# Optimization experiments

Measured on AMD Instinct MI355X. Metric: run time of the kernel, lower is better.

Reference implementation:

```python
import jax, jax.numpy as jnp
import numpy as np

NUM_EMBEDDINGS = 1024
EMBEDDING_DIM = 64
COMMITMENT_COST = 0.25


def setup_inputs() -> dict:
    key = jax.random.key(0)
    k1, k2 = jax.random.split(key)
    inputs = jax.random.normal(k1, (64, 32, 32, EMBEDDING_DIM), dtype=jnp.float32)
    # matches nn.Embedding weight init: uniform(-1/K, 1/K)
    codebook = jax.random.uniform(
        k2, (NUM_EMBEDDINGS, EMBEDDING_DIM), dtype=jnp.float32,
        minval=-1.0 / NUM_EMBEDDINGS, maxval=1.0 / NUM_EMBEDDINGS)
    return {"inputs": inputs, "codebook": codebook}


def reference(inputs, codebook):
    input_shape = inputs.shape
    flat = inputs.reshape(-1, EMBEDDING_DIM)  # [N, D]
    distances = (jnp.sum(flat * flat, axis=1, keepdims=True)
                 + jnp.sum(codebook * codebook, axis=1)
                 - 2.0 * jnp.matmul(flat, codebook.T))
    encoding_indices = jnp.argmin(distances, axis=1)  # [N]
    quantized = codebook[encoding_indices].reshape(input_shape)
    codebook_loss = jnp.mean((jax.lax.stop_gradient(quantized) - inputs) ** 2)
    commitment_loss = jnp.mean((jax.lax.stop_gradient(inputs) - quantized) ** 2)
    vq_loss = codebook_loss + COMMITMENT_COST * commitment_loss
    # straight-through estimator
    quantized_st = inputs + jax.lax.stop_gradient(quantized - inputs)
    return quantized_st, vq_loss
```

## Files before the change

kernel.cpp:

```cpp
#include <hip/hip_runtime.h>

typedef __attribute__((ext_vector_type(8))) short short8;
typedef __attribute__((ext_vector_type(4))) float f32x4;
typedef __attribute__((ext_vector_type(4))) unsigned short u16x4;

#define NVEC 65536
#define DDIM 64
#define KCODES 1024
#define NELEM 4194304
#define VPB 128

static __device__ inline unsigned short f2bf(float f) {
  unsigned u = __builtin_bit_cast(unsigned, f);
  return (unsigned short)((u + 0x7FFFu + ((u >> 16) & 1u)) >> 16);
}
static __device__ inline float bf2f(unsigned short b) {
  return __builtin_bit_cast(float, (unsigned)b << 16);
}

__global__ __launch_bounds__(256) void vq_prep(const float* __restrict__ cb,
                                               unsigned short* __restrict__ cb_bf,
                                               float* __restrict__ en1,
                                               float* __restrict__ out) {
  int t = blockIdx.x * 256 + threadIdx.x;
  float4 v = ((const float4*)cb)[t];
  unsigned short b0 = f2bf(v.x), b1 = f2bf(v.y), b2 = f2bf(v.z), b3 = f2bf(v.w);
  u16x4 pk = {b0, b1, b2, b3};
  *(u16x4*)(cb_bf + (size_t)t * 4) = pk;
  float e0 = bf2f(b0), e1 = bf2f(b1), e2 = bf2f(b2), e3 = bf2f(b3);
  float s = (e0 * e0 + e1 * e1) + (e2 * e2 + e3 * e3);
  s += __shfl_xor(s, 1, 64);
  s += __shfl_xor(s, 2, 64);
  s += __shfl_xor(s, 4, 64);
  s += __shfl_xor(s, 8, 64);
  if ((t & 15) == 0) en1[t >> 4] = 1.0f + s;
  if (t == 0) out[NELEM] = 0.f;
}

__global__ __launch_bounds__(256, 2) void vq_main(
    const float* __restrict__ x, const float* __restrict__ cb,
    const unsigned short* __restrict__ cb_bf, const float* __restrict__ en1,
    float* __restrict__ out) {
  __shared__ float en_s[KCODES];
  __shared__ unsigned skey[VPB];
  __shared__ float xn[VPB];
  __shared__ float wsum[4];

  const int tid = threadIdx.x;
  const int wid = tid >> 6;
  const int L = tid & 63;
  const int c16 = L & 15;
  const int q = L >> 4;
  const int vblk = blockIdx.x * VPB;
  const int mbase = (wid & 1) * 64;
  const int cbase = (wid >> 1) * 512;

  ((float4*)en_s)[tid] = ((const float4*)en1)[tid];
  if (tid < VPB) skey[tid] = 0xFFFFFFFFu;

  short8 a[4][2];
#pragma unroll
  for (int mt = 0; mt < 4; ++mt) {
    const float* xv = x + (size_t)(vblk + mbase + mt * 16 + c16) * DDIM + q * 8;
    float4 u0 = *(const float4*)(xv);
    float4 u1 = *(const float4*)(xv + 4);
    float4 u2 = *(const float4*)(xv + 32);
    float4 u3 = *(const float4*)(xv + 36);
    unsigned short h0 = f2bf(u0.x), h1 = f2bf(u0.y), h2 = f2bf(u0.z), h3 = f2bf(u0.w);
    unsigned short h4 = f2bf(u1.x), h5 = f2bf(u1.y), h6 = f2bf(u1.z), h7 = f2bf(u1.w);
    unsigned short g0 = f2bf(u2.x), g1 = f2bf(u2.y), g2 = f2bf(u2.z), g3 = f2bf(u2.w);
    unsigned short g4 = f2bf(u3.x), g5 = f2bf(u3.y), g6 = f2bf(u3.z), g7 = f2bf(u3.w);
    short8 A0 = {(short)h0, (short)h1, (short)h2, (short)h3,
                 (short)h4, (short)h5, (short)h6, (short)h7};
    short8 A1 = {(short)g0, (short)g1, (short)g2, (short)g3,
                 (short)g4, (short)g5, (short)g6, (short)g7};
    a[mt][0] = A0;
    a[mt][1] = A1;
    float s0 = bf2f(h0), s1 = bf2f(h1), s2 = bf2f(h2), s3 = bf2f(h3);
    float s4 = bf2f(h4), s5 = bf2f(h5), s6 = bf2f(h6), s7 = bf2f(h7);
    float t0 = bf2f(g0), t1 = bf2f(g1), t2 = bf2f(g2), t3 = bf2f(g3);
    float t4 = bf2f(g4), t5 = bf2f(g5), t6 = bf2f(g6), t7 = bf2f(g7);
    float xs = ((s0 * s0 + s1 * s1) + (s2 * s2 + s3 * s3)) +
               ((s4 * s4 + s5 * s5) + (s6 * s6 + s7 * s7)) +
               ((t0 * t0 + t1 * t1) + (t2 * t2 + t3 * t3)) +
               ((t4 * t4 + t5 * t5) + (t6 * t6 + t7 * t7));
    xs += __shfl_xor(xs, 16, 64);
    xs += __shfl_xor(xs, 32, 64);
    if (wid < 2 && L < 16) xn[mbase + mt * 16 + L] = xs;
  }
  __syncthreads();

  unsigned bestk[4][4];
#pragma unroll
  for (int m = 0; m < 4; ++m)
#pragma unroll
    for (int r = 0; r < 4; ++r) bestk[m][r] = 0xFFFFFFFFu;

  const unsigned short* bptr = cb_bf + (size_t)(cbase + c16) * DDIM + q * 8;
#pragma unroll 2
  for (int nt = 0; nt < 32; ++nt) {
    short8 b0 = *(const short8*)(bptr + nt * 16 * DDIM);
    short8 b1 = *(const short8*)(bptr + nt * 16 * DDIM + 32);
    float env = en_s[cbase + nt * 16 + c16];
    unsigned kidx = (unsigned)(cbase + nt * 16 + c16);
#pragma unroll
    for (int m = 0; m < 4; ++m) {
      f32x4 z = {0.f, 0.f, 0.f, 0.f};
      f32x4 acc = __builtin_amdgcn_mfma_f32_16x16x32_bf16(a[m][0], b0, z, 0, 0, 0);
      acc = __builtin_amdgcn_mfma_f32_16x16x32_bf16(a[m][1], b1, acc, 0, 0, 0);
#pragma unroll
      for (int r = 0; r < 4; ++r) {
        float p = fmaf(-2.f, acc[r], env);
        unsigned key = (__builtin_bit_cast(unsigned, p) & 0xFFFFFC00u) | kidx;
        bestk[m][r] = key < bestk[m][r] ? key : bestk[m][r];
      }
    }
  }

#pragma unroll
  for (int m = 0; m < 4; ++m)
#pragma unroll
    for (int r = 0; r < 4; ++r) {
      unsigned k = bestk[m][r];
      k = min(k, (unsigned)__shfl_xor((int)k, 1, 64));
      k = min(k, (unsigned)__shfl_xor((int)k, 2, 64));
      k = min(k, (unsigned)__shfl_xor((int)k, 4, 64));
      k = min(k, (unsigned)__shfl_xor((int)k, 8, 64));
      if (c16 == 0) atomicMin(&skey[mbase + m * 16 + q * 4 + r], k);
    }
  __syncthreads();

#pragma unroll
  for (int i = 0; i < 8; ++i) {
    int f = i * 256 + tid;
    int v = f >> 4, d4 = f & 15;
    int id = (int)(skey[v] & 1023u);
    ((float4*)out)[(size_t)vblk * 16 + f] = ((const float4*)cb)[(size_t)id * 16 + d4];
  }

  float pl = 0.f;
  if (tid < VPB) {
    unsigned k = skey[tid];
    float pt = __builtin_bit_cast(float, k & 0xFFFFFC00u);
    pl = (pt - 1.0f) + xn[tid];
  }
#pragma unroll
  for (int off = 32; off >= 1; off >>= 1) pl += __shfl_down(pl, off, 64);
  if (L == 0) wsum[wid] = pl;
  __syncthreads();
  if (tid == 0)
    atomicAdd(out + NELEM,
              ((wsum[0] + wsum[1]) + (wsum[2] + wsum[3])) * (1.25f / (float)NELEM));
}

extern "C" void kernel_launch(void* const* d_in, const int* in_sizes, int n_in,
                              void* d_out, int out_size, void* d_ws,
                              size_t ws_size, hipStream_t stream) {
  const float* x = (const float*)d_in[0];
  const float* cb = (const float*)d_in[1];
  float* out = (float*)d_out;
  char* ws = (char*)d_ws;
  unsigned short* cb_bf = (unsigned short*)ws;
  float* en1 = (float*)(ws + 131072);

  vq_prep<<<64, 256, 0, stream>>>(cb, cb_bf, en1, out);
  vq_main<<<NVEC / VPB, 256, 0, stream>>>(x, cb, cb_bf, en1, out);
}
```

Measured before the change: 97.34 us.

## Stage pre-swizzled bf16 codebook in LDS with 1024-thread blocks

A new prep kernel writes the bf16 codebook in the exact per-lane MFMA operand order. The main kernel now uses 1024-thread blocks covering 256 vectors each and loads the codebook into LDS in four 256-code stages, so all 16 waves share each global load instead of every wave streaming its half of the codebook from L2. The per-block loss is written to a partial array and summed by a separate small kernel, replacing the global atomicAdd. The cost is two barriers per stage with no double buffering, plus two extra kernel launches.

Result: no change. 97.91 us (+0.6%).

```diff
diff --git a/kernel.cpp b/kernel.cpp
--- a/kernel.cpp
+++ b/kernel.cpp
@@ -8,7 +8,8 @@
 #define DDIM 64
 #define KCODES 1024
 #define NELEM 4194304
-#define VPB 128
+#define VPB 256
+#define NSTAGE 4
 
 static __device__ inline unsigned short f2bf(float f) {
   unsigned u = __builtin_bit_cast(unsigned, f);
@@ -18,29 +19,39 @@
   return __builtin_bit_cast(float, (unsigned)b << 16);
 }
 
-__global__ __launch_bounds__(256) void vq_prep(const float* __restrict__ cb,
-                                               unsigned short* __restrict__ cb_bf,
-                                               float* __restrict__ en1,
-                                               float* __restrict__ out) {
+__global__ __launch_bounds__(256) void vq_prep_en(const float* __restrict__ cb,
+                                                  float* __restrict__ en1) {
   int t = blockIdx.x * 256 + threadIdx.x;
   float4 v = ((const float4*)cb)[t];
-  unsigned short b0 = f2bf(v.x), b1 = f2bf(v.y), b2 = f2bf(v.z), b3 = f2bf(v.w);
-  u16x4 pk = {b0, b1, b2, b3};
-  *(u16x4*)(cb_bf + (size_t)t * 4) = pk;
-  float e0 = bf2f(b0), e1 = bf2f(b1), e2 = bf2f(b2), e3 = bf2f(b3);
+  float e0 = bf2f(f2bf(v.x)), e1 = bf2f(f2bf(v.y));
+  float e2 = bf2f(f2bf(v.z)), e3 = bf2f(f2bf(v.w));
   float s = (e0 * e0 + e1 * e1) + (e2 * e2 + e3 * e3);
   s += __shfl_xor(s, 1, 64);
   s += __shfl_xor(s, 2, 64);
   s += __shfl_xor(s, 4, 64);
   s += __shfl_xor(s, 8, 64);
   if ((t & 15) == 0) en1[t >> 4] = 1.0f + s;
-  if (t == 0) out[NELEM] = 0.f;
-}
-
-__global__ __launch_bounds__(256, 2) void vq_main(
+}
+
+__global__ __launch_bounds__(256) void vq_prep_swz(const float* __restrict__ cb,
+                                                   unsigned short* __restrict__ swz) {
+  int f = blockIdx.x * 256 + threadIdx.x;
+  int lane = f & 63, h = (f >> 6) & 1, gnt = f >> 7;
+  int code = gnt * 16 + (lane & 15);
+  int d = h * 32 + ((lane >> 4) & 3) * 8;
+  const float4* p = (const float4*)(cb + (size_t)code * DDIM + d);
+  float4 u0 = p[0], u1 = p[1];
+  u16x4 p0 = {f2bf(u0.x), f2bf(u0.y), f2bf(u0.z), f2bf(u0.w)};
+  u16x4 p1 = {f2bf(u1.x), f2bf(u1.y), f2bf(u1.z), f2bf(u1.w)};
+  *(u16x4*)(swz + (size_t)f * 8) = p0;
+  *(u16x4*)(swz + (size_t)f * 8 + 4) = p1;
+}
+
+__global__ __launch_bounds__(1024) void vq_main(
     const float* __restrict__ x, const float* __restrict__ cb,
-    const unsigned short* __restrict__ cb_bf, const float* __restrict__ en1,
-    float* __restrict__ out) {
+    const unsigned short* __restrict__ swz, const float* __restrict__ en1,
+    float* __restrict__ out, float* __restrict__ partial) {
+  __shared__ alignas(16) short es[2048 * 8];
   __shared__ float en_s[KCODES];
   __shared__ unsigned skey[VPB];
   __shared__ float xn[VPB];
@@ -52,16 +63,16 @@
   const int c16 = L & 15;
   const int q = L >> 4;
   const int vblk = blockIdx.x * VPB;
-  const int mbase = (wid & 1) * 64;
-  const int cbase = (wid >> 1) * 512;
-
-  ((float4*)en_s)[tid] = ((const float4*)en1)[tid];
+  const int mgrp = wid & 3;
+  const int cq = wid >> 2;
+
+  if (tid < KCODES) en_s[tid] = en1[tid];
   if (tid < VPB) skey[tid] = 0xFFFFFFFFu;
 
   short8 a[4][2];
 #pragma unroll
   for (int mt = 0; mt < 4; ++mt) {
-    const float* xv = x + (size_t)(vblk + mbase + mt * 16 + c16) * DDIM + q * 8;
+    const float* xv = x + (size_t)(vblk + mgrp * 64 + mt * 16 + c16) * DDIM + q * 8;
     float4 u0 = *(const float4*)(xv);
     float4 u1 = *(const float4*)(xv + 4);
     float4 u2 = *(const float4*)(xv + 32);
@@ -78,17 +89,16 @@
     a[mt][1] = A1;
     float s0 = bf2f(h0), s1 = bf2f(h1), s2 = bf2f(h2), s3 = bf2f(h3);
     float s4 = bf2f(h4), s5 = bf2f(h5), s6 = bf2f(h6), s7 = bf2f(h7);
-    float t0 = bf2f(g0), t1 = bf2f(g1), t2 = bf2f(g2), t3 = bf2f(g3);
-    float t4 = bf2f(g4), t5 = bf2f(g5), t6 = bf2f(g6), t7 = bf2f(g7);
-    float xs = ((s0 * s0 + s1 * s1) + (s2 * s2 + s3 * s3)) +
+    float w0 = bf2f(g0), w1 = bf2f(g1), w2 = bf2f(g2), w3 = bf2f(g3);
+    float w4 = bf2f(g4), w5 = bf2f(g5), w6 = bf2f(g6), w7 = bf2f(g7);
+    float sx = ((s0 * s0 + s1 * s1) + (s2 * s2 + s3 * s3)) +
                ((s4 * s4 + s5 * s5) + (s6 * s6 + s7 * s7)) +
-               ((t0 * t0 + t1 * t1) + (t2 * t2 + t3 * t3)) +
-               ((t4 * t4 + t5 * t5) + (t6 * t6 + t7 * t7));
-    xs += __shfl_xor(xs, 16, 64);
-    xs += __shfl_xor(xs, 32, 64);
-    if (wid < 2 && L < 16) xn[mbase + mt * 16 + L] = xs;
-  }
-  __syncthreads();
+               ((w0 * w0 + w1 * w1) + (w2 * w2 + w3 * w3)) +
+               ((w4 * w4 + w5 * w5) + (w6 * w6 + w7 * w7));
+    sx += __shfl_xor(sx, 16, 64);
+    sx += __shfl_xor(sx, 32, 64);
+    if (cq == 0 && L < 16) xn[mgrp * 64 + mt * 16 + L] = sx;
+  }
 
   unsigned bestk[4][4];
 #pragma unroll
@@ -96,23 +106,30 @@
 #pragma unroll
     for (int r = 0; r < 4; ++r) bestk[m][r] = 0xFFFFFFFFu;
 
-  const unsigned short* bptr = cb_bf + (size_t)(cbase + c16) * DDIM + q * 8;
+  for (int s = 0; s < NSTAGE; ++s) {
+    __syncthreads();
+    ((short8*)es)[tid] = ((const short8*)swz)[s * 2048 + tid];
+    ((short8*)es)[tid + 1024] = ((const short8*)swz)[s * 2048 + 1024 + tid];
+    __syncthreads();
+
 #pragma unroll 2
-  for (int nt = 0; nt < 32; ++nt) {
-    short8 b0 = *(const short8*)(bptr + nt * 16 * DDIM);
-    short8 b1 = *(const short8*)(bptr + nt * 16 * DDIM + 32);
-    float env = en_s[cbase + nt * 16 + c16];
-    unsigned kidx = (unsigned)(cbase + nt * 16 + c16);
-#pragma unroll
-    for (int m = 0; m < 4; ++m) {
-      f32x4 z = {0.f, 0.f, 0.f, 0.f};
-      f32x4 acc = __builtin_amdgcn_mfma_f32_16x16x32_bf16(a[m][0], b0, z, 0, 0, 0);
-      acc = __builtin_amdgcn_mfma_f32_16x16x32_bf16(a[m][1], b1, acc, 0, 0, 0);
-#pragma unroll
-      for (int r = 0; r < 4; ++r) {
-        float p = fmaf(-2.f, acc[r], env);
-        unsigned key = (__builtin_bit_cast(unsigned, p) & 0xFFFFFC00u) | kidx;
-        bestk[m][r] = key < bestk[m][r] ? key : bestk[m][r];
+    for (int nt = 0; nt < 4; ++nt) {
+      short8 b0 = ((const short8*)es)[((cq * 4 + nt) * 2 + 0) * 64 + L];
+      short8 b1 = ((const short8*)es)[((cq * 4 + nt) * 2 + 1) * 64 + L];
+      int code0 = s * 256 + cq * 64 + nt * 16;
+      float env = en_s[code0 + c16];
+      unsigned kidx = (unsigned)(code0 + c16);
+#pragma unroll
+      for (int m = 0; m < 4; ++m) {
+        f32x4 z = {0.f, 0.f, 0.f, 0.f};
+        f32x4 acc = __builtin_amdgcn_mfma_f32_16x16x32_bf16(a[m][0], b0, z, 0, 0, 0);
+        acc = __builtin_amdgcn_mfma_f32_16x16x32_bf16(a[m][1], b1, acc, 0, 0, 0);
+#pragma unroll
+        for (int r = 0; r < 4; ++r) {
+          float p = fmaf(-2.f, acc[r], env);
+          unsigned key = (__builtin_bit_cast(unsigned, p) & 0xFFFFFC00u) | kidx;
+          bestk[m][r] = key < bestk[m][r] ? key : bestk[m][r];
+        }
       }
     }
   }
@@ -126,31 +143,43 @@
       k = min(k, (unsigned)__shfl_xor((int)k, 2, 64));
       k = min(k, (unsigned)__shfl_xor((int)k, 4, 64));
       k = min(k, (unsigned)__shfl_xor((int)k, 8, 64));
-      if (c16 == 0) atomicMin(&skey[mbase + m * 16 + q * 4 + r], k);
+      if (c16 == 0) atomicMin(&skey[mgrp * 64 + m * 16 + q * 4 + r], k);
     }
   __syncthreads();
 
 #pragma unroll
-  for (int i = 0; i < 8; ++i) {
-    int f = i * 256 + tid;
+  for (int i = 0; i < 4; ++i) {
+    int f = i * 1024 + tid;
     int v = f >> 4, d4 = f & 15;
     int id = (int)(skey[v] & 1023u);
     ((float4*)out)[(size_t)vblk * 16 + f] = ((const float4*)cb)[(size_t)id * 16 + d4];
   }
 
-  float pl = 0.f;
   if (tid < VPB) {
     unsigned k = skey[tid];
     float pt = __builtin_bit_cast(float, k & 0xFFFFFC00u);
-    pl = (pt - 1.0f) + xn[tid];
-  }
-#pragma unroll
-  for (int off = 32; off >= 1; off >>= 1) pl += __shfl_down(pl, off, 64);
-  if (L == 0) wsum[wid] = pl;
+    float pl = (pt - 1.0f) + xn[tid];
+#pragma unroll
+    for (int off = 32; off >= 1; off >>= 1) pl += __shfl_down(pl, off, 64);
+    if (L == 0) wsum[wid] = pl;
+  }
   __syncthreads();
   if (tid == 0)
-    atomicAdd(out + NELEM,
-              ((wsum[0] + wsum[1]) + (wsum[2] + wsum[3])) * (1.25f / (float)NELEM));
+    partial[blockIdx.x] = (wsum[0] + wsum[1]) + (wsum[2] + wsum[3]);
+}
+
+__global__ __launch_bounds__(256) void vq_loss(const float* __restrict__ partial,
+                                               float* __restrict__ out) {
+  int tid = threadIdx.x;
+  float s = partial[tid];
+#pragma unroll
+  for (int off = 32; off >= 1; off >>= 1) s += __shfl_down(s, off, 64);
+  __shared__ float wsum2[4];
+  if ((tid & 63) == 0) wsum2[tid >> 6] = s;
+  __syncthreads();
+  if (tid == 0)
+    out[NELEM] = ((wsum2[0] + wsum2[1]) + (wsum2[2] + wsum2[3])) *
+                 (1.25f / (float)NELEM);
 }
 
 extern "C" void kernel_launch(void* const* d_in, const int* in_sizes, int n_in,
@@ -160,9 +189,12 @@
   const float* cb = (const float*)d_in[1];
   float* out = (float*)d_out;
   char* ws = (char*)d_ws;
-  unsigned short* cb_bf = (unsigned short*)ws;
+  unsigned short* swz = (unsigned short*)ws;
   float* en1 = (float*)(ws + 131072);
-
-  vq_prep<<<64, 256, 0, stream>>>(cb, cb_bf, en1, out);
-  vq_main<<<NVEC / VPB, 256, 0, stream>>>(x, cb, cb_bf, en1, out);
-}
+  float* partial = (float*)(ws + 135168);
+
+  vq_prep_en<<<64, 256, 0, stream>>>(cb, en1);
+  vq_prep_swz<<<32, 256, 0, stream>>>(cb, swz);
+  vq_main<<<NVEC / VPB, 1024, 0, stream>>>(x, cb, swz, en1, out, partial);
+  vq_loss<<<1, 256, 0, stream>>>(partial, out);
+}
```
